# Kernel tuning notes

Hardware: AMD Instinct MI355X
Metric: run time of the kernel (lower is better)

## Reference

```python
import jax, jax.numpy as jnp
import numpy as np
import math

N = 16
ZIGZAG = np.array([135, 150, 165, 180, 195, 210, 225, 240, 241, 226, 211, 196, 181, 166, 151, 136, 121, 106, 91, 76, 61, 46, 31, 47, 62, 77, 92, 107, 122, 137, 152, 167, 182, 197, 212, 227, 242, 243, 228, 213, 198, 183, 168, 153, 138, 123, 108, 93, 78, 63, 79, 94, 109, 124, 139, 154, 169, 184, 199, 214, 229, 244, 245, 230, 215, 200, 185, 170, 155, 140, 125, 110, 95, 111, 126, 141, 156, 171, 186, 201, 216, 231, 246, 247, 232, 217, 202, 187, 172, 157, 142, 127, 143, 158, 173, 188, 203, 218, 233, 248, 249, 234, 219, 204, 189, 174, 159, 175, 190, 205, 220, 235, 250, 251, 236, 221, 206, 191, 207, 222, 237, 252, 253, 238, 223, 239, 254, 255], dtype=np.int32)

# DCT basis (harmonics) and normalization matrix, matching the torch helpers
_i = np.arange(N, dtype=np.float32)
HARM = np.cos((2.0 * _i[:, None] + 1.0) * (_i[None, :] * math.pi / (2.0 * N))).astype(np.float32)
_n = np.ones((N, 1), dtype=np.float32); _n[0, 0] = 1.0 / math.sqrt(2.0)
NMAT = (_n @ _n.T).astype(np.float32)
SCALE = 1.0 / math.sqrt(2.0 * N)


def setup_inputs() -> dict:
    key = jax.random.key(0)
    x = jax.random.normal(key, (8, 3, 1024, 1024), dtype=jnp.float32)
    return {"x": x}


def reference(x):
    b, c, h, w = x.shape
    # blockify: [b, c, n_blocks, 16, 16], blocks in row-major spatial order
    blocks = x.reshape(b, c, h // N, N, w // N, N).transpose(0, 1, 2, 4, 3, 5).reshape(b, c, -1, N, N)
    harm = jnp.asarray(HARM)
    nmat = jnp.asarray(NMAT)
    # block DCT: scale * n * (H^T @ block @ H)
    coeff = SCALE * nmat * (jnp.matmul(jnp.matmul(harm.T, blocks), harm))
    # zigzag upper-band gather: [b, c, n_blocks, 128]
    flat = coeff.reshape(b, c, -1, N * N)[..., jnp.asarray(ZIGZAG)]
    # adaptive threshold: zero out coefficients below per-block mean
    mean = jnp.mean(flat, axis=3, keepdims=True)
    sel = jnp.where(flat < mean, jnp.float32(0), flat)
    a = jnp.abs(sel) + 1e-12
    # L2 normalize along coefficient dim (torch F.normalize, eps=1e-12)
    norm = jnp.sqrt(jnp.sum(a * a, axis=3, keepdims=True))
    probs = a / jnp.maximum(norm, 1e-12)
    log_prob = jnp.log2(probs)
    entropy = jnp.mean(-jnp.sum(probs * log_prob, axis=3))
    return entropy
```

## Files before the change

### kernel.cpp

```cpp
#include <hip/hip_runtime.h>
#include <math.h>


constexpr double kPi = 3.14159265358979323846;

constexpr double ccos(double x) {
    while (x > kPi) x -= 2.0 * kPi;
    while (x < -kPi) x += 2.0 * kPi;
    double x2 = x * x;
    double term = 1.0, sum = 1.0;
    for (int k = 1; k <= 24; ++k) {
        term *= -x2 / (double)((2 * k - 1) * (2 * k));
        sum += term;
    }
    return sum;
}

struct DctTables {
    float g1[16][16];
    float g2[16][16];
    constexpr DctTables() : g1{}, g2{} {
        for (int j = 0; j < 16; ++j) {
            for (int f = 0; f < 16; ++f) {
                float colf = (float)((double)f * kPi) / 32.0f;
                float arg = (2.0f * (float)j + 1.0f) * colf;
                float h = (float)ccos((double)arg);
                float n = (f == 0) ? 0.70710678118654752440f : 1.0f;
                g1[j][f] = h * n;
                g2[j][f] = h * n * 0.17677669529663688110f;
            }
        }
    }
};
constexpr DctTables kT;

#define NWG 6144
#define NPART (NWG * 4)

#define WAVE_LDS_FENCE() asm volatile("s_waitcnt lgkmcnt(0)" ::: "memory")

__global__ __launch_bounds__(256, 8) void dct_entropy_kernel(
    const float* __restrict__ x, float* __restrict__ partials) {
    __shared__ float smem[4096];

    const int t = threadIdx.x;
    const int wave = t >> 6;
    const int lane = t & 63;
    const int b = lane >> 4;
    const int il = lane & 15;
    float* R = smem + (wave << 10);

    const int g = blockIdx.x;
    const int bc = g >> 8;
    const int br = (g >> 2) & 63;
    const int cg = g & 3;
    const float* base = x + ((size_t)bc << 20) + ((size_t)br << 14) +
                        (cg << 8) + (wave << 6) + (b << 4);

    float xr[16];
    {
        const float* gp = base + (size_t)il * 1024;
#pragma unroll
        for (int c = 0; c < 4; ++c) {
            float4 ld = *(const float4*)(gp + 4 * c);
            xr[4 * c + 0] = ld.x;
            xr[4 * c + 1] = ld.y;
            xr[4 * c + 2] = ld.z;
            xr[4 * c + 3] = ld.w;
        }
    }
    {
        const int cc = (b << 2) + (il >> 2);
        const int lo = il & 3;
#pragma unroll
        for (int v = 0; v < 16; ++v) {
            float acc = 0.0f;
#pragma unroll
            for (int j = 0; j < 16; ++j) acc = fmaf(xr[j], kT.g1[j][v], acc);
            R[(v << 6) + ((cc ^ v) << 2) + lo] = acc;
        }
    }
    WAVE_LDS_FENCE();

    float ti[16];
    {
#pragma unroll
        for (int c = 0; c < 4; ++c) {
            const int ch = (b << 2) + c;
            float4 ld = *(const float4*)(&R[(il << 6) + ((ch ^ il) << 2)]);
            ti[4 * c + 0] = ld.x;
            ti[4 * c + 1] = ld.y;
            ti[4 * c + 2] = ld.z;
            ti[4 * c + 3] = ld.w;
        }
    }
    WAVE_LDS_FENCE();
    {
        const int v = il;
        const int hi = (v > 7) ? 1 : 0;
        const int u_min = 15 - v + hi;
        const int off = hi ? (v * (v - 1) / 2 + 8) : (v * (v + 1) / 2);
        float* wb = &R[b * 136 + off - u_min];
#pragma unroll
        for (int u = 0; u < 16; ++u) {
            float acc = 0.0f;
#pragma unroll
            for (int i = 0; i < 16; ++i) acc = fmaf(ti[i], kT.g2[i][u], acc);
            if (u >= u_min) wb[u] = acc;
        }
    }
    WAVE_LDS_FENCE();

    {
        const int q = lane >> 4;
        const float* C = &R[q * 136 + ((lane & 15) << 3)];
        float4 f0 = *(const float4*)C;
        float4 f1 = *(const float4*)(C + 4);
        float c[8] = {f0.x, f0.y, f0.z, f0.w, f1.x, f1.y, f1.z, f1.w};

        float s = ((c[0] + c[1]) + (c[2] + c[3])) +
                  ((c[4] + c[5]) + (c[6] + c[7]));
#pragma unroll
        for (int m = 1; m <= 8; m <<= 1) s += __shfl_xor(s, m);
        const float mean = s * (1.0f / 128.0f);

        float a[8];
        float sq = 0.0f;
#pragma unroll
        for (int j = 0; j < 8; ++j) {
            a[j] = (c[j] < mean) ? 1e-12f : (fabsf(c[j]) + 1e-12f);
            sq = fmaf(a[j], a[j], sq);
        }
#pragma unroll
        for (int m = 1; m <= 8; m <<= 1) sq += __shfl_xor(sq, m);
        const float inv = 1.0f / fmaxf(sqrtf(sq), 1e-12f);

        float e = 0.0f;
#pragma unroll
        for (int j = 0; j < 8; ++j) {
            float p = a[j] * inv;
            e = fmaf(p, __log2f(p), e);
        }
#pragma unroll
        for (int m = 1; m <= 32; m <<= 1) e += __shfl_xor(e, m);
        if (lane == 0) partials[(g << 2) + wave] = e;
    }
}

__global__ __launch_bounds__(1024) void reduce_partials(
    const float* __restrict__ partials, float* __restrict__ out) {
    __shared__ float s[16];
    float v = 0.0f;
    const float4* p4 = (const float4*)partials;
    for (int i = threadIdx.x; i < NPART / 4; i += 1024) {
        float4 f = p4[i];
        v += (f.x + f.y) + (f.z + f.w);
    }
#pragma unroll
    for (int m = 1; m <= 32; m <<= 1) v += __shfl_xor(v, m);
    if ((threadIdx.x & 63) == 0) s[threadIdx.x >> 6] = v;
    __syncthreads();
    if (threadIdx.x < 16) {
        float tot = s[threadIdx.x];
#pragma unroll
        for (int m = 1; m <= 8; m <<= 1) tot += __shfl_xor(tot, m);
        if (threadIdx.x == 0) out[0] = tot * (-1.0f / 98304.0f);
    }
}

extern "C" void kernel_launch(void* const* d_in, const int* in_sizes, int n_in,
                              void* d_out, int out_size, void* d_ws,
                              size_t ws_size, hipStream_t stream) {
    const float* x = (const float*)d_in[0];
    float* out = (float*)d_out;
    float* ws = (float*)d_ws;
    dct_entropy_kernel<<<NWG, 256, 0, stream>>>(x, ws);
    reduce_partials<<<1, 1024, 0, stream>>>(ws, out);
}
```

Baseline: 144.6 us.

## Coalesce global loads via LDS staging and keep zigzag epilogue in registers

Global input loads are reorganised so each group of 16 lanes reads one contiguous 256-byte row segment, then transposed through swizzled LDS into the per-lane row layout the first DCT pass needs. Previously each lane read 64 bytes from a different row. The second pass no longer scatters zigzag coefficients to LDS and reads them back. Each lane keeps all 16 outputs in registers and masks the entries outside the upper band during the mean, norm and entropy reductions. This trades one extra LDS round trip at load time for better global coalescing and removes one at the end. The cost is more log2 evaluations on masked entries and higher register pressure.

```diff
diff --git a/kernel.cpp b/kernel.cpp
--- a/kernel.cpp
+++ b/kernel.cpp
@@ -54,21 +54,38 @@
     const int bc = g >> 8;
     const int br = (g >> 2) & 63;
     const int cg = g & 3;
-    const float* base = x + ((size_t)bc << 20) + ((size_t)br << 14) +
-                        (cg << 8) + (wave << 6) + (b << 4);
+    const float* gbase =
+        x + ((size_t)bc << 20) + ((size_t)br << 14) + (cg << 8) + (wave << 6);
+
+    float4 v4[4];
+    {
+        const int r0 = lane >> 4;
+        const int ch = lane & 15;
+#pragma unroll
+        for (int k = 0; k < 4; ++k) {
+            v4[k] = *(const float4*)(gbase + (size_t)(4 * k + r0) * 1024 +
+                                     ch * 4);
+        }
+#pragma unroll
+        for (int k = 0; k < 4; ++k) {
+            const int r = 4 * k + r0;
+            *(float4*)(&R[(r << 6) + ((ch ^ r) << 2)]) = v4[k];
+        }
+    }
+    WAVE_LDS_FENCE();
 
     float xr[16];
-    {
-        const float* gp = base + (size_t)il * 1024;
 #pragma unroll
-        for (int c = 0; c < 4; ++c) {
-            float4 ld = *(const float4*)(gp + 4 * c);
-            xr[4 * c + 0] = ld.x;
-            xr[4 * c + 1] = ld.y;
-            xr[4 * c + 2] = ld.z;
-            xr[4 * c + 3] = ld.w;
-        }
+    for (int tt = 0; tt < 4; ++tt) {
+        const int ch = 4 * b + tt;
+        float4 ld = *(const float4*)(&R[(il << 6) + ((ch ^ il) << 2)]);
+        xr[4 * tt + 0] = ld.x;
+        xr[4 * tt + 1] = ld.y;
+        xr[4 * tt + 2] = ld.z;
+        xr[4 * tt + 3] = ld.w;
     }
+    WAVE_LDS_FENCE();
+
     {
         const int cc = (b << 2) + (il >> 2);
         const int lo = il & 3;
@@ -83,68 +100,58 @@
     WAVE_LDS_FENCE();
 
     float ti[16];
-    {
 #pragma unroll
-        for (int c = 0; c < 4; ++c) {
-            const int ch = (b << 2) + c;
-            float4 ld = *(const float4*)(&R[(il << 6) + ((ch ^ il) << 2)]);
-            ti[4 * c + 0] = ld.x;
-            ti[4 * c + 1] = ld.y;
-            ti[4 * c + 2] = ld.z;
-            ti[4 * c + 3] = ld.w;
-        }
-    }
-    WAVE_LDS_FENCE();
-    {
-        const int v = il;
-        const int hi = (v > 7) ? 1 : 0;
-        const int u_min = 15 - v + hi;
-        const int off = hi ? (v * (v - 1) / 2 + 8) : (v * (v + 1) / 2);
-        float* wb = &R[b * 136 + off - u_min];
-#pragma unroll
-        for (int u = 0; u < 16; ++u) {
-            float acc = 0.0f;
-#pragma unroll
-            for (int i = 0; i < 16; ++i) acc = fmaf(ti[i], kT.g2[i][u], acc);
-            if (u >= u_min) wb[u] = acc;
-        }
+    for (int tt = 0; tt < 4; ++tt) {
+        const int ch = 4 * b + tt;
+        float4 ld = *(const float4*)(&R[(il << 6) + ((ch ^ il) << 2)]);
+        ti[4 * tt + 0] = ld.x;
+        ti[4 * tt + 1] = ld.y;
+        ti[4 * tt + 2] = ld.z;
+        ti[4 * tt + 3] = ld.w;
     }
     WAVE_LDS_FENCE();
 
-    {
-        const int q = lane >> 4;
-        const float* C = &R[q * 136 + ((lane & 15) << 3)];
-        float4 f0 = *(const float4*)C;
-        float4 f1 = *(const float4*)(C + 4);
-        float c[8] = {f0.x, f0.y, f0.z, f0.w, f1.x, f1.y, f1.z, f1.w};
+    float c[16];
+#pragma unroll
+    for (int u = 0; u < 16; ++u) {
+        float acc = 0.0f;
+#pragma unroll
+        for (int i = 0; i < 16; ++i) acc = fmaf(ti[i], kT.g2[i][u], acc);
+        c[u] = acc;
+    }
 
-        float s = ((c[0] + c[1]) + (c[2] + c[3])) +
-                  ((c[4] + c[5]) + (c[6] + c[7]));
+    const int v = il;
+    const int u_min = (v > 7) ? (16 - v) : (15 - v);
+
+    float s = 0.0f;
 #pragma unroll
-        for (int m = 1; m <= 8; m <<= 1) s += __shfl_xor(s, m);
-        const float mean = s * (1.0f / 128.0f);
+    for (int u = 0; u < 16; ++u) s += (u >= u_min) ? c[u] : 0.0f;
+#pragma unroll
+    for (int m = 1; m <= 8; m <<= 1) s += __shfl_xor(s, m);
+    const float mean = s * (1.0f / 128.0f);
 
-        float a[8];
-        float sq = 0.0f;
+    float a[16];
+    float sq = 0.0f;
 #pragma unroll
-        for (int j = 0; j < 8; ++j) {
-            a[j] = (c[j] < mean) ? 1e-12f : (fabsf(c[j]) + 1e-12f);
-            sq = fmaf(a[j], a[j], sq);
-        }
+    for (int u = 0; u < 16; ++u) {
+        float au = (c[u] < mean) ? 1e-12f : (fabsf(c[u]) + 1e-12f);
+        a[u] = (u >= u_min) ? au : 0.0f;
+        sq = fmaf(a[u], a[u], sq);
+    }
 #pragma unroll
-        for (int m = 1; m <= 8; m <<= 1) sq += __shfl_xor(sq, m);
-        const float inv = 1.0f / fmaxf(sqrtf(sq), 1e-12f);
+    for (int m = 1; m <= 8; m <<= 1) sq += __shfl_xor(sq, m);
+    const float inv = 1.0f / fmaxf(sqrtf(sq), 1e-12f);
 
-        float e = 0.0f;
+    float e = 0.0f;
 #pragma unroll
-        for (int j = 0; j < 8; ++j) {
-            float p = a[j] * inv;
-            e = fmaf(p, __log2f(p), e);
-        }
+    for (int u = 0; u < 16; ++u) {
+        float p = a[u] * inv;
+        float term = p * __log2f(p);
+        e += (u >= u_min) ? term : 0.0f;
+    }
 #pragma unroll
-        for (int m = 1; m <= 32; m <<= 1) e += __shfl_xor(e, m);
-        if (lane == 0) partials[(g << 2) + wave] = e;
-    }
+    for (int m = 1; m <= 32; m <<= 1) e += __shfl_xor(e, m);
+    if (lane == 0) partials[(g << 2) + wave] = e;
 }
 
 __global__ __launch_bounds__(1024) void reduce_partials(
```

After: 145.4 us. No clear change (+0.6%).
